# Optimization experiments

Hardware: AMD Instinct MI355X
Metric: run time of the kernel (lower is better)

Reference implementation:

```python
import jax, jax.numpy as jnp
import numpy as np

H, N, S, CH, LEN = 512, 64, 512, 1, 4096  # d_model, state size, n_ssm, channels, kernel length


def setup_inputs() -> dict:
    key = jax.random.key(0)
    k1, k2 = jax.random.split(key, 2)
    # dt ~ logUniform(1e-3, 1e-1), standard S4 init
    log_dt = jax.random.uniform(k1, (H,), minval=float(np.log(1e-3)),
                                maxval=float(np.log(1e-1))).astype(jnp.float32)
    # A = -0.5 + i*pi*n (S4D-Lin); stored as inv_A_real = log(-A.real) for real_type='exp'
    inv_A_real = jnp.full((S, N), float(np.log(0.5)), dtype=jnp.float32)
    A_imag = jnp.tile((np.pi * jnp.arange(N, dtype=jnp.float32))[None, :], (S, 1))
    # B = 1 + 0j, stored as real view (..., 2)
    B = jnp.stack([jnp.ones((S, N), jnp.float32), jnp.zeros((S, N), jnp.float32)], axis=-1)
    # C ~ complex normal with std 1/sqrt(2) per component, real view (CH, H, N, 2)
    C = (jax.random.normal(k2, (CH, H, N, 2)) * (0.5 ** 0.5)).astype(jnp.float32)
    return {"log_dt": log_dt, "C": C, "B": B, "inv_A_real": inv_A_real,
            "A_imag": A_imag, "L": LEN}


def _s4d_kernel(log_dt, C, B, inv_A_real, A_imag, L):
    """SSKernelDiag.forward with disc='zoh', real_type='exp', state=None, rate=1.0."""
    dt = jnp.exp(log_dt)                                   # (H,)
    Cc = C[..., 0] + 1j * C[..., 1]                        # (CH, H, N) complex
    Bc = B[..., 0] + 1j * B[..., 1]                        # (S, N) complex
    A = -jnp.exp(inv_A_real) + 1j * A_imag                 # (S, N) complex, Re(A)<0
    rep = H // A.shape[0]
    A = jnp.tile(A, (rep, 1))                              # (H, N)
    Bc = jnp.tile(Bc, (rep, 1))                            # (H, N)
    dtA = A * dt[:, None]                                  # (H, N)
    Cc = Bc[None, :, :] * Cc                               # (CH, H, N)
    Cc = Cc * (jnp.exp(dtA) - 1.0) / A                     # ZOH input discretization
    # log-Vandermonde: K[c,h,l] = 2*Re( sum_n C[c,h,n] * exp(dtA[h,n]*l) )
    ell = jnp.arange(L, dtype=jnp.float32)                 # (L,)
    V = jnp.exp(dtA[:, :, None] * ell)                     # (H, N, L) complex -- the big intermediate
    K = 2.0 * jnp.einsum('chn,hnl->chl', Cc, V).real       # (CH, H, L)
    return K.astype(jnp.float32)


def reference(log_dt, C, B, inv_A_real, A_imag, L):
    # Returns the convolution kernel K of shape (channels, H, L); K_state is None.
    return _s4d_kernel(log_dt, C, B, inv_A_real, A_imag, L)
```

## Files before the change

kernel.cpp:

```cpp
#include <hip/hip_runtime.h>
#include <math.h>

#define H_DIM  512
#define N_DIM  64
#define S_DIM  512
#define L_DIM  4096
#define BLOCK  256
#define KCHUNK 8
#define LSPLIT (L_DIM / (BLOCK * KCHUNK))

__device__ __forceinline__ void cis_big(float th, float l, float& c, float& s) {
    double rev = (double)th * (double)l * 0.15915494309189535;
    rev -= floor(rev);
    float ang = (float)rev * 6.283185307179586f;
    s = __sinf(ang);
    c = __cosf(ang);
}

__global__ __launch_bounds__(BLOCK) void s4d_kernel(
    const float* __restrict__ log_dt,
    const float* __restrict__ C,
    const float* __restrict__ B,
    const float* __restrict__ invA,
    const float* __restrict__ Aim,
    float* __restrict__ out)
{
    __shared__ float lds[N_DIM][8];

    const int h    = blockIdx.x;
    const int half = blockIdx.y;
    const int tid  = threadIdx.x;

    if (tid < N_DIM) {
        const int n  = tid;
        const int s  = h % S_DIM;
        const int sn = s * N_DIM + n;
        const float dt  = __expf(log_dt[h]);
        const float Ar  = -__expf(invA[sn]);
        const float Ai  = Aim[sn];
        const float are = Ar * dt;
        const float aim = Ai * dt;

        const float e1 = __expf(are);
        const float s1 = sinf(aim);
        const float c1 = cosf(aim);
        const float Er = e1 * c1 - 1.0f;
        const float Ei = e1 * s1;

        const float inv = 1.0f / (Ar * Ar + Ai * Ai);
        const float Fr  = (Er * Ar + Ei * Ai) * inv;
        const float Fi  = (Ei * Ar - Er * Ai) * inv;

        const float Br = B[2 * sn], Bi = B[2 * sn + 1];
        const int  chn = h * N_DIM + n;
        const float Cr = C[2 * chn], Ci = C[2 * chn + 1];
        const float BCr = Br * Cr - Bi * Ci;
        const float BCi = Br * Ci + Bi * Cr;
        const float Gr = 2.0f * (BCr * Fr - BCi * Fi);
        const float Gi = 2.0f * (BCr * Fi + BCi * Fr);

        const float eS = __expf(are * (float)BLOCK);
        float cS, sS;
        cis_big(aim, (float)BLOCK, cS, sS);

        lds[n][0] = eS * cS;
        lds[n][1] = eS * sS;
        lds[n][2] = are;
        lds[n][3] = aim;
        lds[n][4] = Gr;
        lds[n][5] = Gi;
    }
    __syncthreads();

    const int   lbase  = half * (BLOCK * KCHUNK) + tid;
    const float lbasef = (float)lbase;

    float acc[KCHUNK];
#pragma unroll
    for (int k = 0; k < KCHUNK; ++k) acc[k] = 0.0f;

    for (int n = 0; n < N_DIM; ++n) {
        const float wr  = lds[n][0];
        const float wi  = lds[n][1];
        const float are = lds[n][2];
        const float aim = lds[n][3];
        const float Gr  = lds[n][4];
        const float Gi  = lds[n][5];

        const float e0 = __expf(are * lbasef);
        float c0, s0;
        cis_big(aim, lbasef, c0, s0);
        float pr = e0 * c0;
        float pi = e0 * s0;

#pragma unroll
        for (int k = 0; k < KCHUNK; ++k) {
            acc[k] = fmaf(Gr, pr, fmaf(-Gi, pi, acc[k]));
            const float t = fmaf(pr, wr, -pi * wi);
            pi = fmaf(pr, wi, pi * wr);
            pr = t;
        }
    }

    float* o = out + h * L_DIM + half * (BLOCK * KCHUNK) + tid;
#pragma unroll
    for (int k = 0; k < KCHUNK; ++k) o[k * BLOCK] = acc[k];
}

extern "C" void kernel_launch(void* const* d_in, const int* in_sizes, int n_in,
                              void* d_out, int out_size, void* d_ws, size_t ws_size,
                              hipStream_t stream) {
    const float* log_dt = (const float*)d_in[0];
    const float* C      = (const float*)d_in[1];
    const float* B      = (const float*)d_in[2];
    const float* invA   = (const float*)d_in[3];
    const float* Aim    = (const float*)d_in[4];
    float* out = (float*)d_out;

    dim3 grid(H_DIM, LSPLIT);
    s4d_kernel<<<grid, BLOCK, 0, stream>>>(log_dt, C, B, invA, Aim, out);
}
```

Baseline: 90.15 us.

## Fold output coefficient into seed and run two recurrence chains per thread

Each block now covers the full length for one h instead of splitting it across two blocks. Each thread seeds two complex-power chains, the second offset by 8*BLOCK, and accumulates only real parts. The output coefficient G is folded into the seed, so the inner loop is a plain add plus a complex rotate. The per-n seed now uses float exp2f, floorf and sincos in place of double-precision range reduction, which cuts transcendental and FP64 work per output. The trade-offs are fewer blocks in the grid and some loss of phase accuracy in the float reduction.

Result: faster. 88.21 us (-2.2%).

```diff
diff --git a/kernel.cpp b/kernel.cpp
--- a/kernel.cpp
+++ b/kernel.cpp
@@ -6,15 +6,13 @@
 #define S_DIM  512
 #define L_DIM  4096
 #define BLOCK  256
-#define KCHUNK 8
-#define LSPLIT (L_DIM / (BLOCK * KCHUNK))
+#define KCH    16
 
 __device__ __forceinline__ void cis_big(float th, float l, float& c, float& s) {
     double rev = (double)th * (double)l * 0.15915494309189535;
     rev -= floor(rev);
     float ang = (float)rev * 6.283185307179586f;
-    s = __sinf(ang);
-    c = __cosf(ang);
+    __sincosf(ang, &s, &c);
 }
 
 __global__ __launch_bounds__(BLOCK) void s4d_kernel(
@@ -25,16 +23,14 @@
     const float* __restrict__ Aim,
     float* __restrict__ out)
 {
-    __shared__ float lds[N_DIM][8];
+    __shared__ float hdr[N_DIM][8];
 
-    const int h    = blockIdx.x;
-    const int half = blockIdx.y;
-    const int tid  = threadIdx.x;
+    const int h   = blockIdx.x;
+    const int tid = threadIdx.x;
 
     if (tid < N_DIM) {
         const int n  = tid;
-        const int s  = h % S_DIM;
-        const int sn = s * N_DIM + n;
+        const int sn = (h % S_DIM) * N_DIM + n;
         const float dt  = __expf(log_dt[h]);
         const float Ar  = -__expf(invA[sn]);
         const float Ai  = Aim[sn];
@@ -59,52 +55,61 @@
         const float Gr = 2.0f * (BCr * Fr - BCi * Fi);
         const float Gi = 2.0f * (BCr * Fi + BCi * Fr);
 
+        float cS, sS, c8, s8;
+        cis_big(aim, (float)BLOCK, cS, sS);
+        cis_big(aim, (float)(8 * BLOCK), c8, s8);
         const float eS = __expf(are * (float)BLOCK);
-        float cS, sS;
-        cis_big(aim, (float)BLOCK, cS, sS);
+        const float e8 = __expf(are * (float)(8 * BLOCK));
 
-        lds[n][0] = eS * cS;
-        lds[n][1] = eS * sS;
-        lds[n][2] = are;
-        lds[n][3] = aim;
-        lds[n][4] = Gr;
-        lds[n][5] = Gi;
+        hdr[n][0] = eS * cS;
+        hdr[n][1] = eS * sS;
+        hdr[n][2] = e8 * c8;
+        hdr[n][3] = e8 * s8;
+        hdr[n][4] = Gr;
+        hdr[n][5] = Gi;
+        hdr[n][6] = are * 1.44269504088896f;
+        hdr[n][7] = aim * 0.15915494309189535f;
     }
     __syncthreads();
 
-    const int   lbase  = half * (BLOCK * KCHUNK) + tid;
-    const float lbasef = (float)lbase;
+    const float l0f = (float)tid;
 
-    float acc[KCHUNK];
+    float acc[KCH];
 #pragma unroll
-    for (int k = 0; k < KCHUNK; ++k) acc[k] = 0.0f;
+    for (int k = 0; k < KCH; ++k) acc[k] = 0.0f;
 
     for (int n = 0; n < N_DIM; ++n) {
-        const float wr  = lds[n][0];
-        const float wi  = lds[n][1];
-        const float are = lds[n][2];
-        const float aim = lds[n][3];
-        const float Gr  = lds[n][4];
-        const float Gi  = lds[n][5];
+        const float4 h0 = *(const float4*)&hdr[n][0];
+        const float4 h1 = *(const float4*)&hdr[n][4];
 
-        const float e0 = __expf(are * lbasef);
-        float c0, s0;
-        cis_big(aim, lbasef, c0, s0);
-        float pr = e0 * c0;
-        float pi = e0 * s0;
+        float rev = h1.w * l0f;
+        rev -= floorf(rev);
+        float s, c;
+        __sincosf(rev * 6.2831853071795864f, &s, &c);
+        const float e0 = exp2f(h1.z * l0f);
+        const float t0 = e0 * c, t1 = e0 * s;
+
+        float ar = fmaf(h1.x, t0, -h1.y * t1);
+        float ai = fmaf(h1.x, t1,  h1.y * t0);
+        float br = fmaf(ar, h0.z, -ai * h0.w);
+        float bi = fmaf(ar, h0.w,  ai * h0.z);
 
 #pragma unroll
-        for (int k = 0; k < KCHUNK; ++k) {
-            acc[k] = fmaf(Gr, pr, fmaf(-Gi, pi, acc[k]));
-            const float t = fmaf(pr, wr, -pi * wi);
-            pi = fmaf(pr, wi, pi * wr);
-            pr = t;
+        for (int k = 0; k < 8; ++k) {
+            acc[k]     += ar;
+            acc[k + 8] += br;
+            const float tA = fmaf(ar, h0.x, -ai * h0.y);
+            ai             = fmaf(ar, h0.y,  ai * h0.x);
+            ar             = tA;
+            const float tB = fmaf(br, h0.x, -bi * h0.y);
+            bi             = fmaf(br, h0.y,  bi * h0.x);
+            br             = tB;
         }
     }
 
-    float* o = out + h * L_DIM + half * (BLOCK * KCHUNK) + tid;
+    float* o = out + h * L_DIM + tid;
 #pragma unroll
-    for (int k = 0; k < KCHUNK; ++k) o[k * BLOCK] = acc[k];
+    for (int k = 0; k < KCH; ++k) o[k * BLOCK] = acc[k];
 }
 
 extern "C" void kernel_launch(void* const* d_in, const int* in_sizes, int n_in,
@@ -117,6 +122,5 @@
     const float* Aim    = (const float*)d_in[4];
     float* out = (float*)d_out;
 
-    dim3 grid(H_DIM, LSPLIT);
-    s4d_kernel<<<grid, BLOCK, 0, stream>>>(log_dt, C, B, invA, Aim, out);
+    s4d_kernel<<<dim3(H_DIM), BLOCK, 0, stream>>>(log_dt, C, B, invA, Aim, out);
 }
```
